# Optimization experiments

Hardware: AMD Instinct MI355X
Metric: run time of the kernel (lower is better)

The kernel has to match this reference:

```python
import jax, jax.numpy as jnp
import numpy as np

B, H, S, DK = 2, 16, 2048, 64


def setup_inputs() -> dict:
    key = jax.random.key(0)
    kq, kk, kv = jax.random.split(key, 3)
    Q = jax.random.normal(kq, (B, H, S, DK), dtype=jnp.float32)
    K = jax.random.normal(kk, (B, H, S, DK), dtype=jnp.float32)
    V = jax.random.normal(kv, (B, H, S, DK), dtype=jnp.float32)
    # causal mask: True = attend, broadcast to [B, H, S, S]
    causal = jnp.tril(jnp.ones((S, S), dtype=jnp.bool_))
    mask = jnp.broadcast_to(causal, (B, H, S, S))
    return {"d_model": 1024, "num_heads": 16, "Q": Q, "K": K, "V": V, "mask": mask}


def reference(d_model, num_heads, Q, K, V, mask):
    dk = Q.shape[-1]
    # scores: [B, H, Sq, Sk] -- naive full materialization, matching the torch code
    scores = jnp.einsum("bhqd,bhkd->bhqk", Q, K) / jnp.sqrt(jnp.asarray(dk, Q.dtype))
    scores = jnp.where(mask, scores, -jnp.inf)
    attn = jax.nn.softmax(scores, axis=-1)
    return jnp.einsum("bhqk,bhkd->bhqd", attn, V)
```

## Files before the change

### kernel.cpp

```cpp
#include <hip/hip_runtime.h>
#include <hip/hip_bf16.h>


using bf16x8 = __attribute__((ext_vector_type(8))) short;
using f32x4  = __attribute__((ext_vector_type(4))) float;
using u32x4  = __attribute__((ext_vector_type(4))) unsigned;
using u32x2  = __attribute__((ext_vector_type(2))) unsigned;

#define SEQ  2048
#define DKK  64
#define KSTR 72

__device__ __forceinline__ short f2bf(float f) {
    union { float f; unsigned u; } v; v.f = f;
    unsigned r = v.u + 0x7fffu + ((v.u >> 16) & 1u);
    return (short)(r >> 16);
}

__device__ __forceinline__ unsigned pkbf(float lo, float hi) {
    union { float f; unsigned u; } a, b; a.f = lo; b.f = hi;
    return __builtin_amdgcn_perm(b.u + 0x8000u, a.u + 0x8000u, 0x07060302u);
}

__device__ __forceinline__ float fexp2(float x) {
#if __has_builtin(__builtin_amdgcn_exp2f)
    return __builtin_amdgcn_exp2f(x);
#else
    return exp2f(x);
#endif
}

__global__ __launch_bounds__(256, 3)
void fa_fwd(const float* __restrict__ Qg, const float* __restrict__ Kg,
            const float* __restrict__ Vg, float* __restrict__ Og) {
    __shared__ short Kt[2][64 * KSTR];
    __shared__ short Vt[2][64 * KSTR];
    __shared__ short Ps[4][16 * KSTR];

    const int qblk = (int)gridDim.x - 1 - (int)blockIdx.x;
    const int bh   = blockIdx.y;
    const int tid  = threadIdx.x;
    const int lane = tid & 63;
    const int w    = tid >> 6;
    const int m16  = lane & 15;
    const int quad = lane >> 4;

    const size_t hoff = (size_t)bh * SEQ * DKK;
    const float* Qh = Qg + hoff;
    const float* Kh = Kg + hoff;
    const float* Vh = Vg + hoff;
    float*       Oh = Og + hoff;

    const int qb   = qblk * 64 + 16 * w;
    const int qrow = qb + m16;

    const int kn = tid >> 2, kc = tid & 3;
    const int vn = (tid & 31) * 2, vd = (tid >> 5) * 8;

    const float cs = 0.18033688011112042f;
    bf16x8 qf[2];
    {
        const float* qp = Qh + (size_t)qrow * DKK + quad * 8;
        #pragma unroll
        for (int h = 0; h < 2; ++h) {
            f32x4 a = *(const f32x4*)(qp + 32 * h);
            f32x4 b = *(const f32x4*)(qp + 32 * h + 4);
            bf16x8 f;
            f[0] = f2bf(a[0] * cs); f[1] = f2bf(a[1] * cs);
            f[2] = f2bf(a[2] * cs); f[3] = f2bf(a[3] * cs);
            f[4] = f2bf(b[0] * cs); f[5] = f2bf(b[1] * cs);
            f[6] = f2bf(b[2] * cs); f[7] = f2bf(b[3] * cs);
            qf[h] = f;
        }
    }

    float mrun = -1e30f, lrun = 0.f;
    f32x4 acc[4];
    {
        f32x4 z = {0.f, 0.f, 0.f, 0.f};
        #pragma unroll
        for (int c = 0; c < 4; ++c) acc[c] = z;
    }

    f32x4 kr[4], vr[4];
    auto load_tile = [&](int kb) {
        const float* kp = Kh + (size_t)(kb + kn) * DKK + kc * 16;
        #pragma unroll
        for (int i = 0; i < 4; ++i) kr[i] = *(const f32x4*)(kp + 4 * i);
        const float* vp = Vh + (size_t)(kb + vn) * DKK + vd;
        vr[0] = *(const f32x4*)vp;         vr[1] = *(const f32x4*)(vp + 4);
        vr[2] = *(const f32x4*)(vp + DKK); vr[3] = *(const f32x4*)(vp + DKK + 4);
    };
    auto store_tile = [&](int buf) {
        u32x4 A, B;
        A[0] = pkbf(kr[0][0], kr[0][1]); A[1] = pkbf(kr[0][2], kr[0][3]);
        A[2] = pkbf(kr[1][0], kr[1][1]); A[3] = pkbf(kr[1][2], kr[1][3]);
        B[0] = pkbf(kr[2][0], kr[2][1]); B[1] = pkbf(kr[2][2], kr[2][3]);
        B[2] = pkbf(kr[3][0], kr[3][1]); B[3] = pkbf(kr[3][2], kr[3][3]);
        *(u32x4*)&Kt[buf][kn * KSTR + kc * 16]     = A;
        *(u32x4*)&Kt[buf][kn * KSTR + kc * 16 + 8] = B;
        #pragma unroll
        for (int i = 0; i < 8; ++i) {
            const float a = (i < 4) ? vr[0][i] : vr[1][i - 4];
            const float b = (i < 4) ? vr[2][i] : vr[3][i - 4];
            *(unsigned*)&Vt[buf][(vd + i) * KSTR + vn] = pkbf(a, b);
        }
    };

    const int T = qblk + 1;
    load_tile(0);
    store_tile(0);
    __syncthreads();

    for (int t = 0; t < T; ++t) {
        const int cur = t & 1;
        const int kb  = t * 64;
        if (t + 1 < T) load_tile((t + 1) * 64);

        f32x4 st[4];
        #pragma unroll
        for (int c = 0; c < 4; ++c) {
            f32x4 z = {0.f, 0.f, 0.f, 0.f};
            const bf16x8 k0 = *(const bf16x8*)&Kt[cur][(16 * c + m16) * KSTR + quad * 8];
            const bf16x8 k1 = *(const bf16x8*)&Kt[cur][(16 * c + m16) * KSTR + 32 + quad * 8];
            z = __builtin_amdgcn_mfma_f32_16x16x32_bf16(k0, qf[0], z, 0, 0, 0);
            z = __builtin_amdgcn_mfma_f32_16x16x32_bf16(k1, qf[1], z, 0, 0, 0);
            st[c] = z;
        }

        float x[16];
        #pragma unroll
        for (int c = 0; c < 4; ++c) {
            #pragma unroll
            for (int r = 0; r < 4; ++r) x[4 * c + r] = st[c][r];
        }
        if (t == T - 1) {
            #pragma unroll
            for (int c = 0; c < 4; ++c) {
                #pragma unroll
                for (int r = 0; r < 4; ++r) {
                    const int n = kb + 16 * c + quad * 4 + r;
                    if (n > qrow) x[4 * c + r] = -1e30f;
                }
            }
        }

        float mx = x[0];
        #pragma unroll
        for (int i = 1; i < 16; ++i) mx = fmaxf(mx, x[i]);
        mx = fmaxf(mx, __shfl_xor(mx, 16));
        mx = fmaxf(mx, __shfl_xor(mx, 32));
        const float mnew  = fmaxf(mrun, mx);
        const float alpha = fexp2(mrun - mnew);
        float p[16], psum = 0.f;
        #pragma unroll
        for (int i = 0; i < 16; ++i) { p[i] = fexp2(x[i] - mnew); psum += p[i]; }
        psum += __shfl_xor(psum, 16);
        psum += __shfl_xor(psum, 32);
        lrun = lrun * alpha + psum;
        mrun = mnew;
        #pragma unroll
        for (int c = 0; c < 4; ++c) {
            #pragma unroll
            for (int r = 0; r < 4; ++r) acc[c][r] *= alpha;
        }

        short* ps = &Ps[w][0];
        #pragma unroll
        for (int c = 0; c < 4; ++c) {
            u32x2 pk;
            pk[0] = pkbf(p[4 * c],     p[4 * c + 1]);
            pk[1] = pkbf(p[4 * c + 2], p[4 * c + 3]);
            *(u32x2*)&ps[m16 * KSTR + 16 * c + quad * 4] = pk;
        }
        __threadfence_block();
        bf16x8 pf[2];
        pf[0] = *(const bf16x8*)&ps[m16 * KSTR + quad * 8];
        pf[1] = *(const bf16x8*)&ps[m16 * KSTR + 32 + quad * 8];

        #pragma unroll
        for (int c = 0; c < 4; ++c) {
            const bf16x8 v0 = *(const bf16x8*)&Vt[cur][(16 * c + m16) * KSTR + quad * 8];
            const bf16x8 v1 = *(const bf16x8*)&Vt[cur][(16 * c + m16) * KSTR + 32 + quad * 8];
            acc[c] = __builtin_amdgcn_mfma_f32_16x16x32_bf16(v0, pf[0], acc[c], 0, 0, 0);
            acc[c] = __builtin_amdgcn_mfma_f32_16x16x32_bf16(v1, pf[1], acc[c], 0, 0, 0);
        }

        if (t + 1 < T) store_tile(cur ^ 1);
        __syncthreads();
    }

    const float inv = 1.0f / lrun;
    float* op = Oh + (size_t)qrow * DKK;
    #pragma unroll
    for (int c = 0; c < 4; ++c) {
        f32x4 o;
        #pragma unroll
        for (int r = 0; r < 4; ++r) o[r] = acc[c][r] * inv;
        *(f32x4*)(op + c * 16 + quad * 4) = o;
    }
}

extern "C" void kernel_launch(void* const* d_in, const int* in_sizes, int n_in,
                              void* d_out, int out_size, void* d_ws, size_t ws_size,
                              hipStream_t stream) {
    const float* Q = (const float*)d_in[2];
    const float* K = (const float*)d_in[3];
    const float* V = (const float*)d_in[4];
    float* O = (float*)d_out;
    (void)in_sizes; (void)n_in; (void)out_size; (void)d_ws; (void)ws_size;
    dim3 grid(SEQ / 64, 32 );
    fa_fwd<<<grid, 256, 0, stream>>>(Q, K, V, O);
}
```

Before: 693.9 us.

## Enlarge query tile to 128 rows per block, two 16-row groups per wave

Each wave now handles 32 query rows, two 16-row MFMA groups, so the block covers 128 queries and each K/V tile loaded into shared memory is reused across twice as many rows. This halves the number of blocks and the per-query K/V global traffic and conversion work. Waves whose rows lie entirely before a key tile skip its compute. Occupancy hint drops to 2 blocks per CU, the grid is halved to 512 blocks with more causal imbalance, and register pressure rises. The exp2 builtin is replaced with exp2f.

```diff
diff --git a/kernel.cpp b/kernel.cpp
--- a/kernel.cpp
+++ b/kernel.cpp
@@ -22,20 +22,12 @@
     return __builtin_amdgcn_perm(b.u + 0x8000u, a.u + 0x8000u, 0x07060302u);
 }
 
-__device__ __forceinline__ float fexp2(float x) {
-#if __has_builtin(__builtin_amdgcn_exp2f)
-    return __builtin_amdgcn_exp2f(x);
-#else
-    return exp2f(x);
-#endif
-}
-
-__global__ __launch_bounds__(256, 3)
+__global__ __launch_bounds__(256, 2)
 void fa_fwd(const float* __restrict__ Qg, const float* __restrict__ Kg,
             const float* __restrict__ Vg, float* __restrict__ Og) {
     __shared__ short Kt[2][64 * KSTR];
     __shared__ short Vt[2][64 * KSTR];
-    __shared__ short Ps[4][16 * KSTR];
+    __shared__ short Ps[4][32 * KSTR];
 
     const int qblk = (int)gridDim.x - 1 - (int)blockIdx.x;
     const int bh   = blockIdx.y;
@@ -51,16 +43,16 @@
     const float* Vh = Vg + hoff;
     float*       Oh = Og + hoff;
 
-    const int qb   = qblk * 64 + 16 * w;
-    const int qrow = qb + m16;
+    const int qb = qblk * 128 + 32 * w;
 
     const int kn = tid >> 2, kc = tid & 3;
     const int vn = (tid & 31) * 2, vd = (tid >> 5) * 8;
 
     const float cs = 0.18033688011112042f;
-    bf16x8 qf[2];
-    {
-        const float* qp = Qh + (size_t)qrow * DKK + quad * 8;
+    bf16x8 qf[2][2];
+    #pragma unroll
+    for (int i = 0; i < 2; ++i) {
+        const float* qp = Qh + (size_t)(qb + 16 * i + m16) * DKK + quad * 8;
         #pragma unroll
         for (int h = 0; h < 2; ++h) {
             f32x4 a = *(const f32x4*)(qp + 32 * h);
@@ -70,16 +62,18 @@
             f[2] = f2bf(a[2] * cs); f[3] = f2bf(a[3] * cs);
             f[4] = f2bf(b[0] * cs); f[5] = f2bf(b[1] * cs);
             f[6] = f2bf(b[2] * cs); f[7] = f2bf(b[3] * cs);
-            qf[h] = f;
-        }
-    }
-
-    float mrun = -1e30f, lrun = 0.f;
-    f32x4 acc[4];
+            qf[i][h] = f;
+        }
+    }
+
+    float mrun[2] = {-1e30f, -1e30f}, lrun[2] = {0.f, 0.f};
+    f32x4 acc[2][4];
     {
         f32x4 z = {0.f, 0.f, 0.f, 0.f};
         #pragma unroll
-        for (int c = 0; c < 4; ++c) acc[c] = z;
+        for (int i = 0; i < 2; ++i)
+            #pragma unroll
+            for (int c = 0; c < 4; ++c) acc[i][c] = z;
     }
 
     f32x4 kr[4], vr[4];
@@ -107,7 +101,7 @@
         }
     };
 
-    const int T = qblk + 1;
+    const int T = 2 * qblk + 2;
     load_tile(0);
     store_tile(0);
     __syncthreads();
@@ -117,87 +111,107 @@
         const int kb  = t * 64;
         if (t + 1 < T) load_tile((t + 1) * 64);
 
-        f32x4 st[4];
-        #pragma unroll
-        for (int c = 0; c < 4; ++c) {
-            f32x4 z = {0.f, 0.f, 0.f, 0.f};
-            const bf16x8 k0 = *(const bf16x8*)&Kt[cur][(16 * c + m16) * KSTR + quad * 8];
-            const bf16x8 k1 = *(const bf16x8*)&Kt[cur][(16 * c + m16) * KSTR + 32 + quad * 8];
-            z = __builtin_amdgcn_mfma_f32_16x16x32_bf16(k0, qf[0], z, 0, 0, 0);
-            z = __builtin_amdgcn_mfma_f32_16x16x32_bf16(k1, qf[1], z, 0, 0, 0);
-            st[c] = z;
-        }
-
-        float x[16];
-        #pragma unroll
-        for (int c = 0; c < 4; ++c) {
-            #pragma unroll
-            for (int r = 0; r < 4; ++r) x[4 * c + r] = st[c][r];
-        }
-        if (t == T - 1) {
+        if (kb <= qb + 31) {
+            bf16x8 kf[4][2];
             #pragma unroll
             for (int c = 0; c < 4; ++c) {
-                #pragma unroll
-                for (int r = 0; r < 4; ++r) {
-                    const int n = kb + 16 * c + quad * 4 + r;
-                    if (n > qrow) x[4 * c + r] = -1e30f;
+                kf[c][0] = *(const bf16x8*)&Kt[cur][(16 * c + m16) * KSTR + quad * 8];
+                kf[c][1] = *(const bf16x8*)&Kt[cur][(16 * c + m16) * KSTR + 32 + quad * 8];
+            }
+            f32x4 st0[4], st1[4];
+            #pragma unroll
+            for (int c = 0; c < 4; ++c) {
+                f32x4 z0 = {0.f, 0.f, 0.f, 0.f}, z1 = {0.f, 0.f, 0.f, 0.f};
+                z0 = __builtin_amdgcn_mfma_f32_16x16x32_bf16(kf[c][0], qf[0][0], z0, 0, 0, 0);
+                z0 = __builtin_amdgcn_mfma_f32_16x16x32_bf16(kf[c][1], qf[0][1], z0, 0, 0, 0);
+                z1 = __builtin_amdgcn_mfma_f32_16x16x32_bf16(kf[c][0], qf[1][0], z1, 0, 0, 0);
+                z1 = __builtin_amdgcn_mfma_f32_16x16x32_bf16(kf[c][1], qf[1][1], z1, 0, 0, 0);
+                st0[c] = z0; st1[c] = z1;
+            }
+
+            const bool domask = (kb + 63 > qb);
+            short* ps = &Ps[w][0];
+
+            #pragma unroll
+            for (int i = 0; i < 2; ++i) {
+                const int qrow = qb + 16 * i + m16;
+                float x[16];
+                #pragma unroll
+                for (int c = 0; c < 4; ++c) {
+                    f32x4 s = i ? st1[c] : st0[c];
+                    #pragma unroll
+                    for (int r = 0; r < 4; ++r) x[4 * c + r] = s[r];
                 }
-            }
-        }
-
-        float mx = x[0];
-        #pragma unroll
-        for (int i = 1; i < 16; ++i) mx = fmaxf(mx, x[i]);
-        mx = fmaxf(mx, __shfl_xor(mx, 16));
-        mx = fmaxf(mx, __shfl_xor(mx, 32));
-        const float mnew  = fmaxf(mrun, mx);
-        const float alpha = fexp2(mrun - mnew);
-        float p[16], psum = 0.f;
-        #pragma unroll
-        for (int i = 0; i < 16; ++i) { p[i] = fexp2(x[i] - mnew); psum += p[i]; }
-        psum += __shfl_xor(psum, 16);
-        psum += __shfl_xor(psum, 32);
-        lrun = lrun * alpha + psum;
-        mrun = mnew;
-        #pragma unroll
-        for (int c = 0; c < 4; ++c) {
-            #pragma unroll
-            for (int r = 0; r < 4; ++r) acc[c][r] *= alpha;
-        }
-
-        short* ps = &Ps[w][0];
-        #pragma unroll
-        for (int c = 0; c < 4; ++c) {
-            u32x2 pk;
-            pk[0] = pkbf(p[4 * c],     p[4 * c + 1]);
-            pk[1] = pkbf(p[4 * c + 2], p[4 * c + 3]);
-            *(u32x2*)&ps[m16 * KSTR + 16 * c + quad * 4] = pk;
-        }
-        __threadfence_block();
-        bf16x8 pf[2];
-        pf[0] = *(const bf16x8*)&ps[m16 * KSTR + quad * 8];
-        pf[1] = *(const bf16x8*)&ps[m16 * KSTR + 32 + quad * 8];
-
-        #pragma unroll
-        for (int c = 0; c < 4; ++c) {
-            const bf16x8 v0 = *(const bf16x8*)&Vt[cur][(16 * c + m16) * KSTR + quad * 8];
-            const bf16x8 v1 = *(const bf16x8*)&Vt[cur][(16 * c + m16) * KSTR + 32 + quad * 8];
-            acc[c] = __builtin_amdgcn_mfma_f32_16x16x32_bf16(v0, pf[0], acc[c], 0, 0, 0);
-            acc[c] = __builtin_amdgcn_mfma_f32_16x16x32_bf16(v1, pf[1], acc[c], 0, 0, 0);
+                if (domask) {
+                    #pragma unroll
+                    for (int c = 0; c < 4; ++c)
+                        #pragma unroll
+                        for (int r = 0; r < 4; ++r) {
+                            const int n = kb + 16 * c + quad * 4 + r;
+                            if (n > qrow) x[4 * c + r] = -1e30f;
+                        }
+                }
+                float mx = x[0];
+                #pragma unroll
+                for (int k = 1; k < 16; ++k) mx = fmaxf(mx, x[k]);
+                mx = fmaxf(mx, __shfl_xor(mx, 16));
+                mx = fmaxf(mx, __shfl_xor(mx, 32));
+                const float mnew  = fmaxf(mrun[i], mx);
+                const float alpha = exp2f(mrun[i] - mnew);
+                float psum = 0.f;
+                #pragma unroll
+                for (int k = 0; k < 16; ++k) { x[k] = exp2f(x[k] - mnew); psum += x[k]; }
+                psum += __shfl_xor(psum, 16);
+                psum += __shfl_xor(psum, 32);
+                lrun[i] = lrun[i] * alpha + psum;
+                mrun[i] = mnew;
+                #pragma unroll
+                for (int c = 0; c < 4; ++c)
+                    #pragma unroll
+                    for (int r = 0; r < 4; ++r) acc[i][c][r] *= alpha;
+                #pragma unroll
+                for (int c = 0; c < 4; ++c) {
+                    u32x2 pk;
+                    pk[0] = pkbf(x[4 * c],     x[4 * c + 1]);
+                    pk[1] = pkbf(x[4 * c + 2], x[4 * c + 3]);
+                    *(u32x2*)&ps[(16 * i + m16) * KSTR + 16 * c + quad * 4] = pk;
+                }
+            }
+            __threadfence_block();
+
+            bf16x8 pf[2][2];
+            #pragma unroll
+            for (int i = 0; i < 2; ++i) {
+                pf[i][0] = *(const bf16x8*)&ps[(16 * i + m16) * KSTR + quad * 8];
+                pf[i][1] = *(const bf16x8*)&ps[(16 * i + m16) * KSTR + 32 + quad * 8];
+            }
+
+            #pragma unroll
+            for (int c = 0; c < 4; ++c) {
+                const bf16x8 v0 = *(const bf16x8*)&Vt[cur][(16 * c + m16) * KSTR + quad * 8];
+                const bf16x8 v1 = *(const bf16x8*)&Vt[cur][(16 * c + m16) * KSTR + 32 + quad * 8];
+                acc[0][c] = __builtin_amdgcn_mfma_f32_16x16x32_bf16(v0, pf[0][0], acc[0][c], 0, 0, 0);
+                acc[0][c] = __builtin_amdgcn_mfma_f32_16x16x32_bf16(v1, pf[0][1], acc[0][c], 0, 0, 0);
+                acc[1][c] = __builtin_amdgcn_mfma_f32_16x16x32_bf16(v0, pf[1][0], acc[1][c], 0, 0, 0);
+                acc[1][c] = __builtin_amdgcn_mfma_f32_16x16x32_bf16(v1, pf[1][1], acc[1][c], 0, 0, 0);
+            }
         }
 
         if (t + 1 < T) store_tile(cur ^ 1);
         __syncthreads();
     }
 
-    const float inv = 1.0f / lrun;
-    float* op = Oh + (size_t)qrow * DKK;
     #pragma unroll
-    for (int c = 0; c < 4; ++c) {
-        f32x4 o;
-        #pragma unroll
-        for (int r = 0; r < 4; ++r) o[r] = acc[c][r] * inv;
-        *(f32x4*)(op + c * 16 + quad * 4) = o;
+    for (int i = 0; i < 2; ++i) {
+        const float inv = 1.0f / lrun[i];
+        float* op = Oh + (size_t)(qb + 16 * i + m16) * DKK;
+        #pragma unroll
+        for (int c = 0; c < 4; ++c) {
+            f32x4 o;
+            #pragma unroll
+            for (int r = 0; r < 4; ++r) o[r] = acc[i][c][r] * inv;
+            *(f32x4*)(op + c * 16 + quad * 4) = o;
+        }
     }
 }
 
@@ -209,6 +223,6 @@
     const float* V = (const float*)d_in[4];
     float* O = (float*)d_out;
     (void)in_sizes; (void)n_in; (void)out_size; (void)d_ws; (void)ws_size;
-    dim3 grid(SEQ / 64, 32 );
+    dim3 grid(SEQ / 128, 32 );
     fa_fwd<<<grid, 256, 0, stream>>>(Q, K, V, O);
 }
```

After: 678.0 us. 1.02x faster.
